# Optimization experiments

Hardware: AMD Instinct MI355X
Metric: run time of the kernel (lower is better)

## Reference

```python
import jax, jax.numpy as jnp
import numpy as np


def _build_masks():
    # pathways_mask: [G genes, P pathways], K genes per pathway (deterministic)
    G, P, K = 5000, 200, 100
    rng = np.random.default_rng(0)
    r = rng.random((G, P))
    pm = np.zeros((G, P), np.float32)
    pm[np.argpartition(r, K, axis=0)[:K], np.arange(P)[None, :]] = 1.0
    l1 = np.maximum(pm.sum(0).astype(np.int64) // 5, 4)   # divide_nodes/min_nodes defaults
    l2 = np.maximum(l1 // 2, 3)
    l3 = np.maximum(l2 // 2, 2)
    g1 = np.repeat(np.arange(P), l1)
    g2 = np.repeat(np.arange(P), l2)
    g3 = np.repeat(np.arange(P), l3)
    # masks stored transposed, [out_features, in_features], as in MaskedLinear buffer
    m1 = np.repeat(pm, l1, axis=1).T                                  # [H1, G]
    m2 = (g2[:, None] == g1[None, :]).astype(np.float32)              # [H2, H1] block-diag repeated
    m3 = (g3[:, None] == g2[None, :]).astype(np.float32)              # [H3, H2]
    m4 = (np.arange(P)[:, None] == g3[None, :]).astype(np.float32)    # [P,  H3] final_mask
    return m1, m2, m3, m4


def setup_inputs():
    B, NL = 8192, 50
    m1, m2, m3, m4 = _build_masks()
    dims = [m1.shape[1], m1.shape[0], m2.shape[0], m3.shape[0], m4.shape[0]]  # [5000,4000,2000,1000,200]
    key = jax.random.key(0)
    ks = iter(jax.random.split(key, 40))
    def W(o, i):
        return jax.random.normal(next(ks), (o, i), jnp.float32) / np.sqrt(i)
    def V(n):
        return jax.random.normal(next(ks), (n,), jnp.float32) * 0.1
    inp = {"x": jax.random.normal(next(ks), (B, dims[0]), jnp.float32)}
    for li, (i, o, m) in enumerate(zip(dims[:4], dims[1:], [m1, m2, m3, m4]), 1):
        inp[f"w{li}"] = W(o, i)
        inp[f"b{li}"] = V(o)
        inp[f"m{li}"] = jnp.asarray(m)
    for li, o in enumerate(dims[1:4], 1):
        inp[f"gamma{li}"] = 1.0 + V(o)
        inp[f"beta{li}"] = V(o)
        inp[f"rm{li}"] = V(o)
        inp[f"rv{li}"] = 0.5 + jax.random.uniform(next(ks), (o,), jnp.float32)
    inp["wc"] = W(NL, dims[4])
    inp["bc"] = V(NL)
    return inp


def _bn_relu(h, gamma, beta, rm, rv):
    # eval-mode BatchNorm1d (running stats) + ReLU; Dropout is identity at eval
    return jax.nn.relu(gamma * (h - rm) * jax.lax.rsqrt(rv + 1e-5) + beta)


def reference(x, w1, b1, m1, w2, b2, m2, w3, b3, m3, w4, b4, m4,
              gamma1, beta1, rm1, rv1, gamma2, beta2, rm2, rv2,
              gamma3, beta3, rm3, rv3, wc, bc):
    h = _bn_relu(x @ (w1 * m1).T + b1, gamma1, beta1, rm1, rv1)
    h = _bn_relu(h @ (w2 * m2).T + b2, gamma2, beta2, rm2, rv2)
    h = _bn_relu(h @ (w3 * m3).T + b3, gamma3, beta3, rm3, rv3)
    scores = jax.nn.relu(h @ (w4 * m4).T + b4)   # [B, n_pathways]
    return scores @ wc.T + bc                    # [B, n_labels]
```

## Files before the change

### kernel.cpp

```cpp
#include <hip/hip_runtime.h>
#include <hip/hip_fp16.h>
#include <stdint.h>

#define GENES 5000
#define NH1   4000
#define NH2   2000
#define NH3   1000
#define NPATH 200
#define NLAB  50
#define NROWS 8192
#define KP    100

typedef _Float16 f16x2 __attribute__((ext_vector_type(2)));
union H2U { unsigned int u; f16x2 v; __half2 h; };

__device__ __forceinline__ float dot2acc(unsigned int a, unsigned int b, float c){
#if __has_builtin(__builtin_amdgcn_fdot2)
    H2U ua; ua.u = a; H2U ub; ub.u = b;
    return __builtin_amdgcn_fdot2(ua.v, ub.v, c, false);
#else
    H2U ua; ua.u = a; H2U ub; ub.u = b;
    float2 fa = __half22float2(ua.h), fb = __half22float2(ub.h);
    return fmaf(fa.x, fb.x, fmaf(fa.y, fb.y, c));
#endif
}

__global__ void k_idx(const float* __restrict__ m1, int* __restrict__ idx1){
    __shared__ int cnt;
    if (threadIdx.x == 0) cnt = 0;
    __syncthreads();
    const float* row = m1 + (size_t)blockIdx.x * 20 * GENES;
    for (int g = threadIdx.x; g < GENES; g += blockDim.x){
        if (row[g] != 0.0f){
            int pos = atomicAdd(&cnt, 1);
            if (pos < KP) idx1[blockIdx.x * KP + pos] = g;
        }
    }
}

__global__ void k_wg1(const float* __restrict__ w1, const float* __restrict__ gamma1,
                      const float* __restrict__ rv1, const int* __restrict__ idx1,
                      __half* __restrict__ wg1p){
    int tid = blockIdx.x * 256 + threadIdx.x;
    if (tid >= 400000) return;
    int kk  = tid / 8000;
    int rem = tid % 8000;
    int c = rem >> 3;
    int e = rem & 7;
    int p = c / 5, g = c % 5;
    int u = e >> 1, kpar = e & 1;
    int k = kk * 2 + kpar;
    int j = p * 20 + g * 4 + u;
    int col = idx1[p * KP + k];
    float a = gamma1[j] * rsqrtf(rv1[j] + 1e-5f);
    wg1p[tid] = (__half)(w1[(size_t)j * GENES + col] * a);
}

__global__ void k_prep(const float* __restrict__ w2, const float* __restrict__ b2,
                       const float* __restrict__ w3, const float* __restrict__ b3,
                       const float* __restrict__ w4, const float* __restrict__ wc,
                       const float* __restrict__ gamma1, const float* __restrict__ beta1,
                       const float* __restrict__ rm1, const float* __restrict__ rv1,
                       const float* __restrict__ gamma2, const float* __restrict__ beta2,
                       const float* __restrict__ rm2, const float* __restrict__ rv2,
                       const float* __restrict__ gamma3, const float* __restrict__ beta3,
                       const float* __restrict__ rm3, const float* __restrict__ rv3,
                       const float* __restrict__ b1,
                       float* __restrict__ bf1, float* __restrict__ wg2, float* __restrict__ bf2,
                       float* __restrict__ wg3, float* __restrict__ bf3,
                       float* __restrict__ wg4, float* __restrict__ wcT){
    int t = blockIdx.x * 256 + threadIdx.x;
    if (t < 40000){
        int k = t / NH2, j = t % NH2, p = j / 10;
        float a = gamma2[j] * rsqrtf(rv2[j] + 1e-5f);
        wg2[t] = w2[(size_t)j * NH1 + 20 * p + k] * a;
    } else if (t < 50000){
        int i = t - 40000;
        int k = i / NH3, j = i % NH3, p = j / 5;
        float a = gamma3[j] * rsqrtf(rv3[j] + 1e-5f);
        wg3[i] = w3[(size_t)j * NH2 + 10 * p + k] * a;
    } else if (t < 51000){
        int i = t - 50000;
        int k = i / NPATH, q = i % NPATH;
        wg4[i] = w4[(size_t)q * NH3 + 5 * q + k];
    } else if (t < 61000){
        int i = t - 51000;
        int q = i / NLAB, n = i % NLAB;
        wcT[i] = wc[(size_t)n * NPATH + q];
    } else if (t < 65000){
        int j = t - 61000;
        float a = gamma1[j] * rsqrtf(rv1[j] + 1e-5f);
        bf1[j] = a * b1[j] + beta1[j] - rm1[j] * a;
    } else if (t < 67000){
        int j = t - 65000;
        float a = gamma2[j] * rsqrtf(rv2[j] + 1e-5f);
        bf2[j] = a * b2[j] + beta2[j] - rm2[j] * a;
    } else if (t < 68000){
        int j = t - 67000;
        float a = gamma3[j] * rsqrtf(rv3[j] + 1e-5f);
        bf3[j] = a * b3[j] + beta3[j] - rm3[j] * a;
    }
}

__global__ __launch_bounds__(256) void k_layer1(const float* __restrict__ x,
        const int* __restrict__ idx1, const __half* __restrict__ wg1p,
        const float* __restrict__ bf1, __half* __restrict__ h1buf){
    __shared__ __align__(16) __half xs[GENES * 4];
    const int r0 = blockIdx.x * 4;
    for (int c = threadIdx.x; c < GENES; c += 256){
        float v0 = x[(size_t)(r0 + 0) * GENES + c];
        float v1 = x[(size_t)(r0 + 1) * GENES + c];
        float v2 = x[(size_t)(r0 + 2) * GENES + c];
        float v3 = x[(size_t)(r0 + 3) * GENES + c];
        __half2* d = (__half2*)(xs + c * 4);
        d[0] = __floats2half2_rn(v0, v1);
        d[1] = __floats2half2_rn(v2, v3);
    }
    __syncthreads();
    const int t = threadIdx.x;
    if (t >= 250) return;
    const int pl = t / 5, g = t % 5;
    for (int pass = 0; pass < 4; ++pass){
        const int p = pass * 50 + pl;
        float acc[4][4];
        #pragma unroll
        for (int u = 0; u < 4; ++u)
            #pragma unroll
            for (int r = 0; r < 4; ++r) acc[u][r] = 0.0f;
        const int2* ip = (const int2*)(idx1 + p * KP);
        const uint4* wp = ((const uint4*)wg1p) + (p * 5 + g);
        for (int kk = 0; kk < 50; ++kk){
            int2 iv = ip[kk];
            uint2 xa = *(const uint2*)(xs + iv.x * 4);
            uint2 xb = *(const uint2*)(xs + iv.y * 4);
            uint4 wv = wp[(size_t)kk * 1000];
            unsigned pr[4];
            pr[0] = (xa.x & 0xffffu) | (xb.x << 16);
            pr[1] = (xa.x >> 16)     | (xb.x & 0xffff0000u);
            pr[2] = (xa.y & 0xffffu) | (xb.y << 16);
            pr[3] = (xa.y >> 16)     | (xb.y & 0xffff0000u);
            const unsigned wu[4] = {wv.x, wv.y, wv.z, wv.w};
            #pragma unroll
            for (int u = 0; u < 4; ++u)
                #pragma unroll
                for (int r = 0; r < 4; ++r)
                    acc[u][r] = dot2acc(pr[r], wu[u], acc[u][r]);
        }
        const float4 bf = ((const float4*)bf1)[p * 5 + g];
        const float bfa[4] = {bf.x, bf.y, bf.z, bf.w};
        const int jb = p * 20 + g * 4;
        #pragma unroll
        for (int r = 0; r < 4; ++r){
            __half2 o01 = __floats2half2_rn(fmaxf(acc[0][r] + bfa[0], 0.0f),
                                            fmaxf(acc[1][r] + bfa[1], 0.0f));
            __half2 o23 = __floats2half2_rn(fmaxf(acc[2][r] + bfa[2], 0.0f),
                                            fmaxf(acc[3][r] + bfa[3], 0.0f));
            uint2 st; st.x = *(unsigned*)&o01; st.y = *(unsigned*)&o23;
            *(uint2*)(h1buf + (size_t)(r0 + r) * NH1 + jb) = st;
        }
    }
}

__global__ __launch_bounds__(256) void k_tail(const __half* __restrict__ h1buf,
        const float* __restrict__ wg2, const float* __restrict__ bf2,
        const float* __restrict__ wg3, const float* __restrict__ bf3,
        const float* __restrict__ wg4, const float* __restrict__ b4,
        const float* __restrict__ wcT, const float* __restrict__ bc,
        float* __restrict__ out){
    __shared__ __align__(16) __half h1s[4 * NH1];
    __shared__ __half h2s[4 * NH2];
    __shared__ __half h3s[4 * NH3];
    __shared__ float  scs[4 * NPATH];
    const int r0 = blockIdx.x * 4;
    {
        const uint4* src = (const uint4*)(h1buf + (size_t)r0 * NH1);
        uint4* dst = (uint4*)h1s;
        for (int i = threadIdx.x; i < 2000; i += 256) dst[i] = src[i];
    }
    __syncthreads();
    for (int j = threadIdx.x; j < NH2; j += 256){
        const int base = (j / 10) * 20;
        float a0 = 0, a1 = 0, a2 = 0, a3 = 0;
        for (int k = 0; k < 20; ++k){
            float w = wg2[k * NH2 + j];
            a0 = fmaf(w, (float)h1s[0 * NH1 + base + k], a0);
            a1 = fmaf(w, (float)h1s[1 * NH1 + base + k], a1);
            a2 = fmaf(w, (float)h1s[2 * NH1 + base + k], a2);
            a3 = fmaf(w, (float)h1s[3 * NH1 + base + k], a3);
        }
        float b = bf2[j];
        h2s[0 * NH2 + j] = (__half)fmaxf(a0 + b, 0.0f);
        h2s[1 * NH2 + j] = (__half)fmaxf(a1 + b, 0.0f);
        h2s[2 * NH2 + j] = (__half)fmaxf(a2 + b, 0.0f);
        h2s[3 * NH2 + j] = (__half)fmaxf(a3 + b, 0.0f);
    }
    __syncthreads();
    for (int j = threadIdx.x; j < NH3; j += 256){
        const int base = (j / 5) * 10;
        float a0 = 0, a1 = 0, a2 = 0, a3 = 0;
        for (int k = 0; k < 10; ++k){
            float w = wg3[k * NH3 + j];
            a0 = fmaf(w, (float)h2s[0 * NH2 + base + k], a0);
            a1 = fmaf(w, (float)h2s[1 * NH2 + base + k], a1);
            a2 = fmaf(w, (float)h2s[2 * NH2 + base + k], a2);
            a3 = fmaf(w, (float)h2s[3 * NH2 + base + k], a3);
        }
        float b = bf3[j];
        h3s[0 * NH3 + j] = (__half)fmaxf(a0 + b, 0.0f);
        h3s[1 * NH3 + j] = (__half)fmaxf(a1 + b, 0.0f);
        h3s[2 * NH3 + j] = (__half)fmaxf(a2 + b, 0.0f);
        h3s[3 * NH3 + j] = (__half)fmaxf(a3 + b, 0.0f);
    }
    __syncthreads();
    if (threadIdx.x < NPATH){
        const int j = threadIdx.x;
        const int base = 5 * j;
        float a0 = 0, a1 = 0, a2 = 0, a3 = 0;
        for (int k = 0; k < 5; ++k){
            float w = wg4[k * NPATH + j];
            a0 = fmaf(w, (float)h3s[0 * NH3 + base + k], a0);
            a1 = fmaf(w, (float)h3s[1 * NH3 + base + k], a1);
            a2 = fmaf(w, (float)h3s[2 * NH3 + base + k], a2);
            a3 = fmaf(w, (float)h3s[3 * NH3 + base + k], a3);
        }
        float b = b4[j];
        scs[0 * NPATH + j] = fmaxf(a0 + b, 0.0f);
        scs[1 * NPATH + j] = fmaxf(a1 + b, 0.0f);
        scs[2 * NPATH + j] = fmaxf(a2 + b, 0.0f);
        scs[3 * NPATH + j] = fmaxf(a3 + b, 0.0f);
    }
    __syncthreads();
    if (threadIdx.x < 200){
        const int r = threadIdx.x / NLAB, n = threadIdx.x % NLAB;
        float acc = bc[n];
        const float* sp = scs + r * NPATH;
        for (int q = 0; q < NPATH; ++q)
            acc = fmaf(sp[q], wcT[q * NLAB + n], acc);
        out[(size_t)(r0 + r) * NLAB + n] = acc;
    }
}

extern "C" void kernel_launch(void* const* d_in, const int* in_sizes, int n_in,
                              void* d_out, int out_size, void* d_ws, size_t ws_size,
                              hipStream_t stream){
    (void)in_sizes; (void)n_in; (void)out_size; (void)ws_size;
    const float* x      = (const float*)d_in[0];
    const float* w1     = (const float*)d_in[1];
    const float* b1     = (const float*)d_in[2];
    const float* m1     = (const float*)d_in[3];
    const float* w2     = (const float*)d_in[4];
    const float* b2     = (const float*)d_in[5];
    const float* w3     = (const float*)d_in[7];
    const float* b3     = (const float*)d_in[8];
    const float* w4     = (const float*)d_in[10];
    const float* b4     = (const float*)d_in[11];
    const float* gamma1 = (const float*)d_in[13];
    const float* beta1  = (const float*)d_in[14];
    const float* rm1    = (const float*)d_in[15];
    const float* rv1    = (const float*)d_in[16];
    const float* gamma2 = (const float*)d_in[17];
    const float* beta2  = (const float*)d_in[18];
    const float* rm2    = (const float*)d_in[19];
    const float* rv2    = (const float*)d_in[20];
    const float* gamma3 = (const float*)d_in[21];
    const float* beta3  = (const float*)d_in[22];
    const float* rm3    = (const float*)d_in[23];
    const float* rv3    = (const float*)d_in[24];
    const float* wc     = (const float*)d_in[25];
    const float* bc     = (const float*)d_in[26];

    char* ws = (char*)d_ws;
    size_t off = 0;
    __half* h1buf = (__half*)(ws + off); off += (size_t)NROWS * NH1 * 2;
    int*    idx1  = (int*)  (ws + off);  off += (size_t)NPATH * KP * 4;
    __half* wg1p  = (__half*)(ws + off); off += (size_t)400000 * 2;
    float*  bf1   = (float*)(ws + off);  off += (size_t)NH1 * 4;
    float*  wg2   = (float*)(ws + off);  off += (size_t)40000 * 4;
    float*  bf2   = (float*)(ws + off);  off += (size_t)NH2 * 4;
    float*  wg3   = (float*)(ws + off);  off += (size_t)10000 * 4;
    float*  bf3   = (float*)(ws + off);  off += (size_t)NH3 * 4;
    float*  wg4   = (float*)(ws + off);  off += (size_t)1000 * 4;
    float*  wcT   = (float*)(ws + off);  off += (size_t)10000 * 4;

    hipLaunchKernelGGL(k_idx,    dim3(NPATH),    dim3(256), 0, stream, m1, idx1);
    hipLaunchKernelGGL(k_wg1,    dim3(1563),     dim3(256), 0, stream, w1, gamma1, rv1, idx1, wg1p);
    hipLaunchKernelGGL(k_prep,   dim3(266),      dim3(256), 0, stream,
                       w2, b2, w3, b3, w4, wc,
                       gamma1, beta1, rm1, rv1, gamma2, beta2, rm2, rv2,
                       gamma3, beta3, rm3, rv3, b1,
                       bf1, wg2, bf2, wg3, bf3, wg4, wcT);
    hipLaunchKernelGGL(k_layer1, dim3(NROWS/4),  dim3(256), 0, stream, x, idx1, wg1p, bf1, h1buf);
    hipLaunchKernelGGL(k_tail,   dim3(NROWS/4),  dim3(256), 0, stream,
                       h1buf, wg2, bf2, wg3, bf3, wg4, b4, wcT, bc, (float*)d_out);
}
```

Baseline: 568.0 us.

## Pack per-pathway tail weights in registers and software-pipeline layer1 loads

The tail kernel is restructured so each thread owns one pathway. It keeps that pathway's fp16 layer2/3/4 weights (packed by k_prep into 256 halves per pathway) in registers and computes all three layers with dot2, using no shared-memory intermediate layers and no barriers between them. Each tail block now handles 8 rows and stages the classifier weights in LDS. Layer1 gains double-buffered prefetch of its index and weight loads, plus perm-based half packing. The risks are high register pressure from the 128-entry per-thread array, only 200 of 256 threads active in the tail, and fp16 rounding of the tail weights.

```diff
diff --git a/kernel.cpp b/kernel.cpp
--- a/kernel.cpp
+++ b/kernel.cpp
@@ -22,6 +22,21 @@
     H2U ua; ua.u = a; H2U ub; ub.u = b;
     float2 fa = __half22float2(ua.h), fb = __half22float2(ub.h);
     return fmaf(fa.x, fb.x, fmaf(fa.y, fb.y, c));
+#endif
+}
+
+__device__ __forceinline__ unsigned pklo(unsigned xa, unsigned xb){
+#if __has_builtin(__builtin_amdgcn_perm)
+    return __builtin_amdgcn_perm(xb, xa, 0x05040100u);
+#else
+    return (xa & 0xffffu) | (xb << 16);
+#endif
+}
+__device__ __forceinline__ unsigned pkhi(unsigned xa, unsigned xb){
+#if __has_builtin(__builtin_amdgcn_perm)
+    return __builtin_amdgcn_perm(xb, xa, 0x07060302u);
+#else
+    return (xa >> 16) | (xb & 0xffff0000u);
 #endif
 }
 
@@ -66,37 +81,44 @@
                        const float* __restrict__ gamma3, const float* __restrict__ beta3,
                        const float* __restrict__ rm3, const float* __restrict__ rv3,
                        const float* __restrict__ b1,
-                       float* __restrict__ bf1, float* __restrict__ wg2, float* __restrict__ bf2,
-                       float* __restrict__ wg3, float* __restrict__ bf3,
-                       float* __restrict__ wg4, float* __restrict__ wcT){
+                       float* __restrict__ bf1, float* __restrict__ bf2,
+                       float* __restrict__ bf3,
+                       __half* __restrict__ wpk, float* __restrict__ wcT){
     int t = blockIdx.x * 256 + threadIdx.x;
     if (t < 40000){
-        int k = t / NH2, j = t % NH2, p = j / 10;
+        int p = t / 200, i = t % 200;
+        int u2 = i / 20, k = i % 20;
+        int j = 10 * p + u2;
         float a = gamma2[j] * rsqrtf(rv2[j] + 1e-5f);
-        wg2[t] = w2[(size_t)j * NH1 + 20 * p + k] * a;
+        wpk[p * 256 + i] = (__half)(w2[(size_t)j * NH1 + 20 * p + k] * a);
     } else if (t < 50000){
-        int i = t - 40000;
-        int k = i / NH3, j = i % NH3, p = j / 5;
+        int i2 = t - 40000;
+        int p = i2 / 50, i = i2 % 50;
+        int u3 = i / 10, k = i % 10;
+        int j = 5 * p + u3;
         float a = gamma3[j] * rsqrtf(rv3[j] + 1e-5f);
-        wg3[i] = w3[(size_t)j * NH2 + 10 * p + k] * a;
+        wpk[p * 256 + 200 + i] = (__half)(w3[(size_t)j * NH2 + 10 * p + k] * a);
     } else if (t < 51000){
-        int i = t - 50000;
-        int k = i / NPATH, q = i % NPATH;
-        wg4[i] = w4[(size_t)q * NH3 + 5 * q + k];
-    } else if (t < 61000){
-        int i = t - 51000;
+        int i2 = t - 50000;
+        int p = i2 / 5, k = i2 % 5;
+        wpk[p * 256 + 250 + k] = (__half)(w4[(size_t)p * NH3 + 5 * p + k]);
+    } else if (t < 51200){
+        int p = t - 51000;
+        wpk[p * 256 + 255] = (__half)0.0f;
+    } else if (t < 61200){
+        int i = t - 51200;
         int q = i / NLAB, n = i % NLAB;
         wcT[i] = wc[(size_t)n * NPATH + q];
-    } else if (t < 65000){
-        int j = t - 61000;
+    } else if (t < 65200){
+        int j = t - 61200;
         float a = gamma1[j] * rsqrtf(rv1[j] + 1e-5f);
         bf1[j] = a * b1[j] + beta1[j] - rm1[j] * a;
-    } else if (t < 67000){
-        int j = t - 65000;
+    } else if (t < 67200){
+        int j = t - 65200;
         float a = gamma2[j] * rsqrtf(rv2[j] + 1e-5f);
         bf2[j] = a * b2[j] + beta2[j] - rm2[j] * a;
-    } else if (t < 68000){
-        int j = t - 67000;
+    } else if (t < 68200){
+        int j = t - 67200;
         float a = gamma3[j] * rsqrtf(rv3[j] + 1e-5f);
         bf3[j] = a * b3[j] + beta3[j] - rm3[j] * a;
     }
@@ -128,23 +150,40 @@
             #pragma unroll
             for (int r = 0; r < 4; ++r) acc[u][r] = 0.0f;
         const int2* ip = (const int2*)(idx1 + p * KP);
-        const uint4* wp = ((const uint4*)wg1p) + (p * 5 + g);
-        for (int kk = 0; kk < 50; ++kk){
-            int2 iv = ip[kk];
-            uint2 xa = *(const uint2*)(xs + iv.x * 4);
-            uint2 xb = *(const uint2*)(xs + iv.y * 4);
-            uint4 wv = wp[(size_t)kk * 1000];
-            unsigned pr[4];
-            pr[0] = (xa.x & 0xffffu) | (xb.x << 16);
-            pr[1] = (xa.x >> 16)     | (xb.x & 0xffff0000u);
-            pr[2] = (xa.y & 0xffffu) | (xb.y << 16);
-            pr[3] = (xa.y >> 16)     | (xb.y & 0xffff0000u);
-            const unsigned wu[4] = {wv.x, wv.y, wv.z, wv.w};
-            #pragma unroll
-            for (int u = 0; u < 4; ++u)
+        const char* wb = (const char*)(((const uint4*)wg1p) + (p * 5 + g));
+        int2 ivA = ip[0], ivB = ip[1];
+        uint4 wvA = *(const uint4*)wb;
+        uint4 wvB = *(const uint4*)(wb + 16000);
+        for (int kk = 0; kk < 50; kk += 2){
+            const int nk = (kk + 2 < 50) ? kk + 2 : 0;
+            int2 ivA2 = ip[nk], ivB2 = ip[nk + 1];
+            uint4 wvA2 = *(const uint4*)(wb + (size_t)nk * 16000);
+            uint4 wvB2 = *(const uint4*)(wb + (size_t)(nk + 1) * 16000);
+            {
+                uint2 xa = *(const uint2*)(xs + ivA.x * 4);
+                uint2 xb = *(const uint2*)(xs + ivA.y * 4);
+                unsigned pr[4] = { pklo(xa.x, xb.x), pkhi(xa.x, xb.x),
+                                   pklo(xa.y, xb.y), pkhi(xa.y, xb.y) };
+                const unsigned wu[4] = {wvA.x, wvA.y, wvA.z, wvA.w};
                 #pragma unroll
-                for (int r = 0; r < 4; ++r)
-                    acc[u][r] = dot2acc(pr[r], wu[u], acc[u][r]);
+                for (int u = 0; u < 4; ++u)
+                    #pragma unroll
+                    for (int r = 0; r < 4; ++r)
+                        acc[u][r] = dot2acc(pr[r], wu[u], acc[u][r]);
+            }
+            {
+                uint2 xa = *(const uint2*)(xs + ivB.x * 4);
+                uint2 xb = *(const uint2*)(xs + ivB.y * 4);
+                unsigned pr[4] = { pklo(xa.x, xb.x), pkhi(xa.x, xb.x),
+                                   pklo(xa.y, xb.y), pkhi(xa.y, xb.y) };
+                const unsigned wu[4] = {wvB.x, wvB.y, wvB.z, wvB.w};
+                #pragma unroll
+                for (int u = 0; u < 4; ++u)
+                    #pragma unroll
+                    for (int r = 0; r < 4; ++r)
+                        acc[u][r] = dot2acc(pr[r], wu[u], acc[u][r]);
+            }
+            ivA = ivA2; ivB = ivB2; wvA = wvA2; wvB = wvB2;
         }
         const float4 bf = ((const float4*)bf1)[p * 5 + g];
         const float bfa[4] = {bf.x, bf.y, bf.z, bf.w};
@@ -162,80 +201,76 @@
 }
 
 __global__ __launch_bounds__(256) void k_tail(const __half* __restrict__ h1buf,
-        const float* __restrict__ wg2, const float* __restrict__ bf2,
-        const float* __restrict__ wg3, const float* __restrict__ bf3,
-        const float* __restrict__ wg4, const float* __restrict__ b4,
+        const __half* __restrict__ wpk, const float* __restrict__ bf2,
+        const float* __restrict__ bf3, const float* __restrict__ b4,
         const float* __restrict__ wcT, const float* __restrict__ bc,
         float* __restrict__ out){
-    __shared__ __align__(16) __half h1s[4 * NH1];
-    __shared__ __half h2s[4 * NH2];
-    __shared__ __half h3s[4 * NH3];
-    __shared__ float  scs[4 * NPATH];
-    const int r0 = blockIdx.x * 4;
-    {
-        const uint4* src = (const uint4*)(h1buf + (size_t)r0 * NH1);
-        uint4* dst = (uint4*)h1s;
-        for (int i = threadIdx.x; i < 2000; i += 256) dst[i] = src[i];
+    __shared__ float scs[8 * NPATH];
+    __shared__ __align__(16) float wcs[NPATH * NLAB];
+    const int t = threadIdx.x;
+    const int r0 = blockIdx.x * 8;
+    for (int i = t; i < (NPATH * NLAB) / 4; i += 256)
+        ((float4*)wcs)[i] = ((const float4*)wcT)[i];
+    if (t < NPATH){
+        const int p = t;
+        unsigned cw[128];
+        const uint4* wp4 = (const uint4*)(wpk + p * 256);
+        #pragma unroll
+        for (int i = 0; i < 32; ++i){
+            uint4 v = wp4[i];
+            cw[4*i] = v.x; cw[4*i+1] = v.y; cw[4*i+2] = v.z; cw[4*i+3] = v.w;
+        }
+        float c2[10], c3[5];
+        #pragma unroll
+        for (int i = 0; i < 10; ++i) c2[i] = bf2[10 * p + i];
+        #pragma unroll
+        for (int i = 0; i < 5; ++i)  c3[i] = bf3[5 * p + i];
+        const float b4p = b4[p];
+        for (int r = 0; r < 8; ++r){
+            const uint2* hp = (const uint2*)(h1buf + (size_t)(r0 + r) * NH1 + 20 * p);
+            unsigned h1u[10];
+            #pragma unroll
+            for (int i = 0; i < 5; ++i){ uint2 v = hp[i]; h1u[2*i] = v.x; h1u[2*i+1] = v.y; }
+            unsigned h2u[5];
+            #pragma unroll
+            for (int i = 0; i < 5; ++i){
+                float a0 = c2[2*i], a1 = c2[2*i+1];
+                #pragma unroll
+                for (int kk = 0; kk < 10; ++kk){
+                    a0 = dot2acc(h1u[kk], cw[(2*i) * 10 + kk], a0);
+                    a1 = dot2acc(h1u[kk], cw[(2*i+1) * 10 + kk], a1);
+                }
+                __half2 hh = __floats2half2_rn(fmaxf(a0, 0.f), fmaxf(a1, 0.f));
+                h2u[i] = *(unsigned*)&hh;
+            }
+            float h3f[5];
+            #pragma unroll
+            for (int u = 0; u < 5; ++u){
+                float a = c3[u];
+                #pragma unroll
+                for (int kk = 0; kk < 5; ++kk)
+                    a = dot2acc(h2u[kk], cw[100 + u * 5 + kk], a);
+                h3f[u] = fmaxf(a, 0.f);
+            }
+            unsigned h3u[3];
+            __half2 t01 = __floats2half2_rn(h3f[0], h3f[1]); h3u[0] = *(unsigned*)&t01;
+            __half2 t23 = __floats2half2_rn(h3f[2], h3f[3]); h3u[1] = *(unsigned*)&t23;
+            __half2 t4  = __floats2half2_rn(h3f[4], 0.f);    h3u[2] = *(unsigned*)&t4;
+            float a = b4p;
+            #pragma unroll
+            for (int kk = 0; kk < 3; ++kk)
+                a = dot2acc(h3u[kk], cw[125 + kk], a);
+            scs[r * NPATH + p] = fmaxf(a, 0.f);
+        }
     }
     __syncthreads();
-    for (int j = threadIdx.x; j < NH2; j += 256){
-        const int base = (j / 10) * 20;
-        float a0 = 0, a1 = 0, a2 = 0, a3 = 0;
-        for (int k = 0; k < 20; ++k){
-            float w = wg2[k * NH2 + j];
-            a0 = fmaf(w, (float)h1s[0 * NH1 + base + k], a0);
-            a1 = fmaf(w, (float)h1s[1 * NH1 + base + k], a1);
-            a2 = fmaf(w, (float)h1s[2 * NH1 + base + k], a2);
-            a3 = fmaf(w, (float)h1s[3 * NH1 + base + k], a3);
-        }
-        float b = bf2[j];
-        h2s[0 * NH2 + j] = (__half)fmaxf(a0 + b, 0.0f);
-        h2s[1 * NH2 + j] = (__half)fmaxf(a1 + b, 0.0f);
-        h2s[2 * NH2 + j] = (__half)fmaxf(a2 + b, 0.0f);
-        h2s[3 * NH2 + j] = (__half)fmaxf(a3 + b, 0.0f);
-    }
-    __syncthreads();
-    for (int j = threadIdx.x; j < NH3; j += 256){
-        const int base = (j / 5) * 10;
-        float a0 = 0, a1 = 0, a2 = 0, a3 = 0;
-        for (int k = 0; k < 10; ++k){
-            float w = wg3[k * NH3 + j];
-            a0 = fmaf(w, (float)h2s[0 * NH2 + base + k], a0);
-            a1 = fmaf(w, (float)h2s[1 * NH2 + base + k], a1);
-            a2 = fmaf(w, (float)h2s[2 * NH2 + base + k], a2);
-            a3 = fmaf(w, (float)h2s[3 * NH2 + base + k], a3);
-        }
-        float b = bf3[j];
-        h3s[0 * NH3 + j] = (__half)fmaxf(a0 + b, 0.0f);
-        h3s[1 * NH3 + j] = (__half)fmaxf(a1 + b, 0.0f);
-        h3s[2 * NH3 + j] = (__half)fmaxf(a2 + b, 0.0f);
-        h3s[3 * NH3 + j] = (__half)fmaxf(a3 + b, 0.0f);
-    }
-    __syncthreads();
-    if (threadIdx.x < NPATH){
-        const int j = threadIdx.x;
-        const int base = 5 * j;
-        float a0 = 0, a1 = 0, a2 = 0, a3 = 0;
-        for (int k = 0; k < 5; ++k){
-            float w = wg4[k * NPATH + j];
-            a0 = fmaf(w, (float)h3s[0 * NH3 + base + k], a0);
-            a1 = fmaf(w, (float)h3s[1 * NH3 + base + k], a1);
-            a2 = fmaf(w, (float)h3s[2 * NH3 + base + k], a2);
-            a3 = fmaf(w, (float)h3s[3 * NH3 + base + k], a3);
-        }
-        float b = b4[j];
-        scs[0 * NPATH + j] = fmaxf(a0 + b, 0.0f);
-        scs[1 * NPATH + j] = fmaxf(a1 + b, 0.0f);
-        scs[2 * NPATH + j] = fmaxf(a2 + b, 0.0f);
-        scs[3 * NPATH + j] = fmaxf(a3 + b, 0.0f);
-    }
-    __syncthreads();
-    if (threadIdx.x < 200){
-        const int r = threadIdx.x / NLAB, n = threadIdx.x % NLAB;
+    for (int o = t; o < 8 * NLAB; o += 256){
+        int r = o / NLAB, n = o % NLAB;
         float acc = bc[n];
         const float* sp = scs + r * NPATH;
+        #pragma unroll 8
         for (int q = 0; q < NPATH; ++q)
-            acc = fmaf(sp[q], wcT[q * NLAB + n], acc);
+            acc = fmaf(sp[q], wcs[q * NLAB + n], acc);
         out[(size_t)(r0 + r) * NLAB + n] = acc;
     }
 }
@@ -275,21 +310,19 @@
     int*    idx1  = (int*)  (ws + off);  off += (size_t)NPATH * KP * 4;
     __half* wg1p  = (__half*)(ws + off); off += (size_t)400000 * 2;
     float*  bf1   = (float*)(ws + off);  off += (size_t)NH1 * 4;
-    float*  wg2   = (float*)(ws + off);  off += (size_t)40000 * 4;
     float*  bf2   = (float*)(ws + off);  off += (size_t)NH2 * 4;
-    float*  wg3   = (float*)(ws + off);  off += (size_t)10000 * 4;
     float*  bf3   = (float*)(ws + off);  off += (size_t)NH3 * 4;
-    float*  wg4   = (float*)(ws + off);  off += (size_t)1000 * 4;
-    float*  wcT   = (float*)(ws + off);  off += (size_t)10000 * 4;
-
-    hipLaunchKernelGGL(k_idx,    dim3(NPATH),    dim3(256), 0, stream, m1, idx1);
-    hipLaunchKernelGGL(k_wg1,    dim3(1563),     dim3(256), 0, stream, w1, gamma1, rv1, idx1, wg1p);
-    hipLaunchKernelGGL(k_prep,   dim3(266),      dim3(256), 0, stream,
+    __half* wpk   = (__half*)(ws + off); off += (size_t)NPATH * 256 * 2;
+    float*  wcT   = (float*)(ws + off);  off += (size_t)NPATH * NLAB * 4;
+
+    hipLaunchKernelGGL(k_idx,    dim3(NPATH),   dim3(256), 0, stream, m1, idx1);
+    hipLaunchKernelGGL(k_wg1,    dim3(1563),    dim3(256), 0, stream, w1, gamma1, rv1, idx1, wg1p);
+    hipLaunchKernelGGL(k_prep,   dim3(267),     dim3(256), 0, stream,
                        w2, b2, w3, b3, w4, wc,
                        gamma1, beta1, rm1, rv1, gamma2, beta2, rm2, rv2,
                        gamma3, beta3, rm3, rv3, b1,
-                       bf1, wg2, bf2, wg3, bf3, wg4, wcT);
-    hipLaunchKernelGGL(k_layer1, dim3(NROWS/4),  dim3(256), 0, stream, x, idx1, wg1p, bf1, h1buf);
-    hipLaunchKernelGGL(k_tail,   dim3(NROWS/4),  dim3(256), 0, stream,
-                       h1buf, wg2, bf2, wg3, bf3, wg4, b4, wcT, bc, (float*)d_out);
-}
+                       bf1, bf2, bf3, wpk, wcT);
+    hipLaunchKernelGGL(k_layer1, dim3(NROWS/4), dim3(256), 0, stream, x, idx1, wg1p, bf1, h1buf);
+    hipLaunchKernelGGL(k_tail,   dim3(NROWS/8), dim3(256), 0, stream,
+                       h1buf, wpk, bf2, bf3, b4, wcT, bc, (float*)d_out);
+}
```

Result: faster. 538.6 us (-5.2%).
